# Kernel optimization log

Measured on AMD Instinct MI355X. Metric: run time of the kernel, lower is better.

## Reference

```python
import jax, jax.numpy as jnp
import numpy as np

# dims
B, C, H, W = 2, 64, 512, 512
T = 16                      # tile_size_l0
GH, GW = H // T, W // T
K = GH * GW                 # 1024 tiles
KMAX = 256                  # kmax_l0
HID = 2 * C
# routing config
THRESH = 0.0                # theta_on
TEMP = 1.0                  # gate_temperature
C_HEAVY, C_CHEAP = 1.0, 0.1
BUDGET_TOTAL = 512.0        # per-sample budget
MU = 1.0                    # dual controller multiplier (mu_init)


def setup_inputs() -> dict:
    key = jax.random.key(0)
    ks = jax.random.split(key, 6)
    sc = 0.05
    return {
        "dense_features": jax.random.normal(ks[0], (B, C, H, W), jnp.float32),
        "utility_logits": jax.random.normal(ks[1], (B, K), jnp.float32),
        "W1": jax.random.normal(ks[2], (C, HID), jnp.float32) * sc,
        "b1": jnp.zeros((HID,), jnp.float32),
        "W2": jax.random.normal(ks[3], (HID, C), jnp.float32) * sc,
        "b2": jnp.zeros((C,), jnp.float32),
        "Wa": jax.random.normal(ks[4], (C,), jnp.float32) * sc,
        "ba": jnp.zeros((1,), jnp.float32),
    }


def _select_mask(u):
    # vectorized equivalent of _select_from_gate: gate = u >= thresh,
    # keep top-KMAX gated tiles per sample ordered by utility.
    gate = u >= THRESH
    masked = jnp.where(gate, u, -1e30)
    vals, idx = jax.lax.top_k(masked, KMAX)          # [B,KMAX]
    valid = vals > -1e29
    rows = jnp.arange(u.shape[0])[:, None]
    return jnp.zeros(u.shape, bool).at[rows, idx].set(valid)  # [B,K]


def reference(dense_features, utility_logits, W1, b1, W2, b2, Wa, ba):
    x, u = dense_features, utility_logits
    # ste_gate_from_utilities (threshold mode)
    probabilities = jax.nn.sigmoid((u - THRESH) / TEMP)
    hard = (u >= THRESH).astype(x.dtype)
    gates = hard + probabilities - jax.lax.stop_gradient(probabilities)  # STE
    # tile selection (detached, like gates[b].detach())
    sel = _select_mask(jax.lax.stop_gradient(u))                 # [B,K]
    mask = sel.reshape(B, GH, GW).astype(x.dtype)
    mask = jnp.repeat(jnp.repeat(mask, T, axis=1), T, axis=2)[:, None]  # [B,1,H,W]
    # heavy path: pointwise channel MLP -> detail, alpha blend on selected tiles
    h = jax.nn.gelu(jnp.einsum('bchw,cd->bdhw', x, W1) + b1[None, :, None, None])
    detail = jnp.einsum('bdhw,dc->bchw', h, W2) + b2[None, :, None, None]
    alpha = jax.nn.sigmoid(jnp.einsum('bchw,c->bhw', x, Wa) + ba[0])[:, None]  # [B,1,H,W]
    alpha_out = mask * alpha
    detail_out = mask * detail
    heavy = x + alpha_out * detail
    # budget controller
    expected_cost = jnp.sum(probabilities * C_HEAVY + (1.0 - probabilities) * C_CHEAP)
    budget_loss = MU * jax.nn.relu(expected_cost - BUDGET_TOTAL * B)
    return heavy, detail_out, alpha_out, probabilities, gates, expected_cost, budget_loss
```

## Files before the change

kernel.cpp:

```cpp
#include <hip/hip_runtime.h>
#include <math.h>

#define Bv 2
#define Cv 64
#define Hv 512
#define Wv 512
#define Tv 16
#define Kv 1024
#define KMAXv 256
#define HIDv 128
#define HWv (Hv * Wv)

#define OFF_HEAVY 0
#define OFF_DETAIL 33554432
#define OFF_ALPHA 67108864
#define OFF_PROB 67633152
#define OFF_GATES 67635200
#define OFF_EC 67637248
#define OFF_BL 67637249

#define WS_SEL_OFF 0
#define WS_COST_OFF 8192

__global__ __launch_bounds__(1024) void sel_kernel(const float* __restrict__ u,
                                                   float* __restrict__ out,
                                                   int* __restrict__ selflag,
                                                   float* __restrict__ costp) {
    int b = blockIdx.x;
    int t = threadIdx.x;
    __shared__ float us[Kv];
    __shared__ float red[16];

    float ui = u[b * Kv + t];
    us[t] = ui;
    __syncthreads();

    float p = 1.0f / (1.0f + __expf(-ui));
    float hard = (ui >= 0.0f) ? 1.0f : 0.0f;
    out[OFF_PROB + b * Kv + t] = p;
    out[OFF_GATES + b * Kv + t] = (hard + p) - p;

    float cost = p + (1.0f - p) * 0.1f;
    #pragma unroll
    for (int o = 32; o > 0; o >>= 1) cost += __shfl_down(cost, o, 64);
    int wave = t >> 6, lane = t & 63;
    if (lane == 0) red[wave] = cost;
    __syncthreads();
    if (t == 0) {
        float s = 0.f;
        #pragma unroll
        for (int i = 0; i < 16; i++) s += red[i];
        costp[b] = s;
    }

    int selected = 0;
    if (ui >= 0.0f) {
        int r = 0;
        for (int j = 0; j < Kv; j += 4) {
            float4 uj = *(const float4*)&us[j];
            r += (uj.x > ui) || (uj.x == ui && (j + 0) < t);
            r += (uj.y > ui) || (uj.y == ui && (j + 1) < t);
            r += (uj.z > ui) || (uj.z == ui && (j + 2) < t);
            r += (uj.w > ui) || (uj.w == ui && (j + 3) < t);
        }
        selected = (r < KMAXv) ? 1 : 0;
    }
    selflag[b * Kv + t] = selected;
}

__global__ __launch_bounds__(256) void copy_kernel(const float* __restrict__ x,
                                                   float* __restrict__ out,
                                                   const int* __restrict__ selflag,
                                                   const float* __restrict__ costp) {
    int blk = blockIdx.x;
    int t = threadIdx.x;

    if (blk == 0 && t == 0) {
        float ec = costp[0] + costp[1];
        out[OFF_EC] = ec;
        out[OFF_BL] = (ec > 1024.0f) ? (ec - 1024.0f) : 0.0f;
    }

    if (selflag[blk]) return;

    int b = blk >> 10;
    int tile = blk & 1023;
    int gh = tile >> 5, gw = tile & 31;
    int h0 = gh * Tv, w0 = gw * Tv;

    int cplane = t >> 6;
    int r = (t >> 2) & 15;
    int q = t & 3;
    int base = ((b * Cv + cplane) * Hv + (h0 + r)) * Wv + w0 + q * 4;
    float4 z = make_float4(0.f, 0.f, 0.f, 0.f);
    #pragma unroll 4
    for (int c4 = 0; c4 < 16; c4++) {
        int idx = base + c4 * 4 * HWv;
        float4 v = *(const float4*)&x[idx];
        *(float4*)&out[OFF_HEAVY + idx] = v;
        *(float4*)&out[OFF_DETAIL + idx] = z;
    }
    if (t < 64) {
        int r2 = t >> 2, q2 = t & 3;
        int aidx = (b * Hv + h0 + r2) * Wv + w0 + q2 * 4;
        *(float4*)&out[OFF_ALPHA + aidx] = z;
    }
}

__global__ __launch_bounds__(256) void mlp_kernel(const float* __restrict__ x,
                                                  const float* __restrict__ W1,
                                                  const float* __restrict__ b1,
                                                  const float* __restrict__ W2,
                                                  const float* __restrict__ b2,
                                                  const float* __restrict__ Wa,
                                                  const float* __restrict__ ba,
                                                  float* __restrict__ out,
                                                  const int* __restrict__ selflag) {
    int blk = blockIdx.x;
    if (!selflag[blk]) return;

    __shared__ float xs[Cv][257];
    int t = threadIdx.x;
    int b = blk >> 10;
    int tile = blk & 1023;
    int gh = tile >> 5, gw = tile & 31;
    int h0 = gh * Tv, w0 = gw * Tv;

    int pr = t >> 4, pc = t & 15;
    int pbase = ((b * Cv) * Hv + (h0 + pr)) * Wv + w0 + pc;

    #pragma unroll 8
    for (int c = 0; c < Cv; c++) xs[c][t] = x[pbase + c * HWv];
    __syncthreads();

    float aacc = ba[0];
    #pragma unroll 8
    for (int c = 0; c < Cv; c++) aacc += xs[c][t] * Wa[c];
    float alpha = 1.0f / (1.0f + __expf(-aacc));
    out[OFF_ALPHA + (b * Hv + h0 + pr) * Wv + w0 + pc] = alpha;

    float D[Cv];
    #pragma unroll
    for (int c4 = 0; c4 < 16; c4++) {
        float4 bb = *(const float4*)&b2[c4 * 4];
        D[4 * c4 + 0] = bb.x; D[4 * c4 + 1] = bb.y;
        D[4 * c4 + 2] = bb.z; D[4 * c4 + 3] = bb.w;
    }

    for (int d0 = 0; d0 < HIDv; d0 += 32) {
        float Hc[32];
        #pragma unroll
        for (int j4 = 0; j4 < 8; j4++) {
            float4 bb = *(const float4*)&b1[d0 + 4 * j4];
            Hc[4 * j4 + 0] = bb.x; Hc[4 * j4 + 1] = bb.y;
            Hc[4 * j4 + 2] = bb.z; Hc[4 * j4 + 3] = bb.w;
        }
        #pragma unroll 2
        for (int c = 0; c < Cv; c++) {
            float xc = xs[c][t];
            const float4* w1p = (const float4*)(W1 + c * HIDv + d0);
            #pragma unroll
            for (int j4 = 0; j4 < 8; j4++) {
                float4 w = w1p[j4];
                Hc[4 * j4 + 0] += xc * w.x;
                Hc[4 * j4 + 1] += xc * w.y;
                Hc[4 * j4 + 2] += xc * w.z;
                Hc[4 * j4 + 3] += xc * w.w;
            }
        }
        #pragma unroll
        for (int j = 0; j < 32; j++) {
            float zv = Hc[j];
            float zz = 0.7978845608028654f * (zv + 0.044715f * zv * zv * zv);
            float e = __expf(2.0f * zz);
            float th = 1.0f - 2.0f / (e + 1.0f);
            Hc[j] = 0.5f * zv * (1.0f + th);
        }
        #pragma unroll 2
        for (int j = 0; j < 32; j++) {
            float hj = Hc[j];
            const float4* w2p = (const float4*)(W2 + (d0 + j) * Cv);
            #pragma unroll
            for (int c4 = 0; c4 < 16; c4++) {
                float4 w = w2p[c4];
                D[4 * c4 + 0] += hj * w.x;
                D[4 * c4 + 1] += hj * w.y;
                D[4 * c4 + 2] += hj * w.z;
                D[4 * c4 + 3] += hj * w.w;
            }
        }
    }

    #pragma unroll 4
    for (int c = 0; c < Cv; c++) {
        int idx = pbase + c * HWv;
        float det = D[c];
        out[OFF_DETAIL + idx] = det;
        out[OFF_HEAVY + idx] = xs[c][t] + alpha * det;
    }
}

extern "C" void kernel_launch(void* const* d_in, const int* in_sizes, int n_in,
                              void* d_out, int out_size, void* d_ws, size_t ws_size,
                              hipStream_t stream) {
    const float* x  = (const float*)d_in[0];
    const float* u  = (const float*)d_in[1];
    const float* W1 = (const float*)d_in[2];
    const float* b1 = (const float*)d_in[3];
    const float* W2 = (const float*)d_in[4];
    const float* b2 = (const float*)d_in[5];
    const float* Wa = (const float*)d_in[6];
    const float* ba = (const float*)d_in[7];
    float* out = (float*)d_out;

    char* ws = (char*)d_ws;
    int*   selflag = (int*)(ws + WS_SEL_OFF);
    float* costp   = (float*)(ws + WS_COST_OFF);

    sel_kernel<<<Bv, 1024, 0, stream>>>(u, out, selflag, costp);
    copy_kernel<<<Bv * Kv, 256, 0, stream>>>(x, out, selflag, costp);
    mlp_kernel<<<Bv * Kv, 256, 0, stream>>>(x, W1, b1, W2, b2, Wa, ba, out, selflag);
}
```

Measured before the change: 708.2 us.

## Fuse copy and MLP kernels into one launch over 8x32 half-tile-pair blocks

Merges the passthrough copy kernel and the MLP kernel into a single kernel. Each block now covers an 8-row by 32-column region spanning two horizontally adjacent tiles, so row accesses are wider and more coalesced. Mixed regions compute the MLP for every pixel and mask the outputs per tile. Shared-memory staging of x is replaced by re-reading x from global memory (through the cache) three times, and occupancy is hinted with launch_bounds(256,4). The cost is wasted MLP work on unselected halves of mixed pairs, plus extra global reads.

```diff
diff --git a/kernel.cpp b/kernel.cpp
--- a/kernel.cpp
+++ b/kernel.cpp
@@ -5,7 +5,6 @@
 #define Cv 64
 #define Hv 512
 #define Wv 512
-#define Tv 16
 #define Kv 1024
 #define KMAXv 256
 #define HIDv 128
@@ -68,10 +67,16 @@
     selflag[b * Kv + t] = selected;
 }
 
-__global__ __launch_bounds__(256) void copy_kernel(const float* __restrict__ x,
-                                                   float* __restrict__ out,
-                                                   const int* __restrict__ selflag,
-                                                   const float* __restrict__ costp) {
+__global__ __launch_bounds__(256, 4) void fused_kernel(const float* __restrict__ x,
+                                                       const float* __restrict__ W1,
+                                                       const float* __restrict__ b1,
+                                                       const float* __restrict__ W2,
+                                                       const float* __restrict__ b2,
+                                                       const float* __restrict__ Wa,
+                                                       const float* __restrict__ ba,
+                                                       float* __restrict__ out,
+                                                       const int* __restrict__ selflag,
+                                                       const float* __restrict__ costp) {
     int blk = blockIdx.x;
     int t = threadIdx.x;
 
@@ -81,63 +86,56 @@
         out[OFF_BL] = (ec > 1024.0f) ? (ec - 1024.0f) : 0.0f;
     }
 
-    if (selflag[blk]) return;
-
     int b = blk >> 10;
-    int tile = blk & 1023;
-    int gh = tile >> 5, gw = tile & 31;
-    int h0 = gh * Tv, w0 = gw * Tv;
-
-    int cplane = t >> 6;
-    int r = (t >> 2) & 15;
-    int q = t & 3;
-    int base = ((b * Cv + cplane) * Hv + (h0 + r)) * Wv + w0 + q * 4;
-    float4 z = make_float4(0.f, 0.f, 0.f, 0.f);
-    #pragma unroll 4
-    for (int c4 = 0; c4 < 16; c4++) {
-        int idx = base + c4 * 4 * HWv;
-        float4 v = *(const float4*)&x[idx];
-        *(float4*)&out[OFF_HEAVY + idx] = v;
-        *(float4*)&out[OFF_DETAIL + idx] = z;
-    }
-    if (t < 64) {
-        int r2 = t >> 2, q2 = t & 3;
-        int aidx = (b * Hv + h0 + r2) * Wv + w0 + q2 * 4;
-        *(float4*)&out[OFF_ALPHA + aidx] = z;
-    }
-}
-
-__global__ __launch_bounds__(256) void mlp_kernel(const float* __restrict__ x,
-                                                  const float* __restrict__ W1,
-                                                  const float* __restrict__ b1,
-                                                  const float* __restrict__ W2,
-                                                  const float* __restrict__ b2,
-                                                  const float* __restrict__ Wa,
-                                                  const float* __restrict__ ba,
-                                                  float* __restrict__ out,
-                                                  const int* __restrict__ selflag) {
-    int blk = blockIdx.x;
-    if (!selflag[blk]) return;
-
-    __shared__ float xs[Cv][257];
-    int t = threadIdx.x;
-    int b = blk >> 10;
-    int tile = blk & 1023;
-    int gh = tile >> 5, gw = tile & 31;
-    int h0 = gh * Tv, w0 = gw * Tv;
-
-    int pr = t >> 4, pc = t & 15;
-    int pbase = ((b * Cv) * Hv + (h0 + pr)) * Wv + w0 + pc;
-
-    #pragma unroll 8
-    for (int c = 0; c < Cv; c++) xs[c][t] = x[pbase + c * HWv];
-    __syncthreads();
+    int rem = blk & 1023;
+    int pairid = rem >> 1;
+    int half = rem & 1;
+    int gh = pairid >> 4;
+    int gp = pairid & 15;
+    int h0 = gh * 16 + half * 8;
+    int w0 = gp * 32;
+
+    int tA = b * Kv + gh * 32 + gp * 2;
+    int selA = selflag[tA];
+    int selB = selflag[tA + 1];
+
+    if ((selA | selB) == 0) {
+        int pl = t >> 6;
+        int r = (t >> 3) & 7;
+        int q = t & 7;
+        int base = ((b * Cv + pl) * Hv + h0 + r) * Wv + w0 + q * 4;
+        float4 z = make_float4(0.f, 0.f, 0.f, 0.f);
+        #pragma unroll 4
+        for (int it = 0; it < 16; it++) {
+            int idx = base + it * 4 * HWv;
+            float4 v = *(const float4*)&x[idx];
+            *(float4*)&out[OFF_HEAVY + idx] = v;
+            *(float4*)&out[OFF_DETAIL + idx] = z;
+        }
+        if (t < 64) {
+            int r2 = t >> 3, q2 = t & 7;
+            int aidx = (b * Hv + h0 + r2) * Wv + w0 + q2 * 4;
+            *(float4*)&out[OFF_ALPHA + aidx] = z;
+        }
+        return;
+    }
+
+    int r = t >> 5;
+    int cc = t & 31;
+    float msk = (cc < 16) ? (float)selA : (float)selB;
+    int pbase = (b * Cv * Hv + h0 + r) * Wv + w0 + cc;
 
     float aacc = ba[0];
-    #pragma unroll 8
-    for (int c = 0; c < Cv; c++) aacc += xs[c][t] * Wa[c];
+    for (int c0 = 0; c0 < Cv; c0 += 8) {
+        float xv[8];
+        #pragma unroll
+        for (int k = 0; k < 8; k++) xv[k] = x[pbase + (c0 + k) * HWv];
+        #pragma unroll
+        for (int k = 0; k < 8; k++) aacc += xv[k] * Wa[c0 + k];
+    }
     float alpha = 1.0f / (1.0f + __expf(-aacc));
-    out[OFF_ALPHA + (b * Hv + h0 + pr) * Wv + w0 + pc] = alpha;
+    float am = msk * alpha;
+    out[OFF_ALPHA + (b * Hv + h0 + r) * Wv + w0 + cc] = am;
 
     float D[Cv];
     #pragma unroll
@@ -155,17 +153,22 @@
             Hc[4 * j4 + 0] = bb.x; Hc[4 * j4 + 1] = bb.y;
             Hc[4 * j4 + 2] = bb.z; Hc[4 * j4 + 3] = bb.w;
         }
-        #pragma unroll 2
-        for (int c = 0; c < Cv; c++) {
-            float xc = xs[c][t];
-            const float4* w1p = (const float4*)(W1 + c * HIDv + d0);
+        for (int c0 = 0; c0 < Cv; c0 += 8) {
+            float xv[8];
             #pragma unroll
-            for (int j4 = 0; j4 < 8; j4++) {
-                float4 w = w1p[j4];
-                Hc[4 * j4 + 0] += xc * w.x;
-                Hc[4 * j4 + 1] += xc * w.y;
-                Hc[4 * j4 + 2] += xc * w.z;
-                Hc[4 * j4 + 3] += xc * w.w;
+            for (int k = 0; k < 8; k++) xv[k] = x[pbase + (c0 + k) * HWv];
+            #pragma unroll
+            for (int k = 0; k < 8; k++) {
+                float xc = xv[k];
+                const float4* w1p = (const float4*)(W1 + (c0 + k) * HIDv + d0);
+                #pragma unroll
+                for (int j4 = 0; j4 < 8; j4++) {
+                    float4 w = w1p[j4];
+                    Hc[4 * j4 + 0] += xc * w.x;
+                    Hc[4 * j4 + 1] += xc * w.y;
+                    Hc[4 * j4 + 2] += xc * w.z;
+                    Hc[4 * j4 + 3] += xc * w.w;
+                }
             }
         }
         #pragma unroll
@@ -176,7 +179,7 @@
             float th = 1.0f - 2.0f / (e + 1.0f);
             Hc[j] = 0.5f * zv * (1.0f + th);
         }
-        #pragma unroll 2
+        #pragma unroll 4
         for (int j = 0; j < 32; j++) {
             float hj = Hc[j];
             const float4* w2p = (const float4*)(W2 + (d0 + j) * Cv);
@@ -191,12 +194,17 @@
         }
     }
 
-    #pragma unroll 4
-    for (int c = 0; c < Cv; c++) {
-        int idx = pbase + c * HWv;
-        float det = D[c];
-        out[OFF_DETAIL + idx] = det;
-        out[OFF_HEAVY + idx] = xs[c][t] + alpha * det;
+    for (int c0 = 0; c0 < Cv; c0 += 8) {
+        float xv[8];
+        #pragma unroll
+        for (int k = 0; k < 8; k++) xv[k] = x[pbase + (c0 + k) * HWv];
+        #pragma unroll
+        for (int k = 0; k < 8; k++) {
+            int idx = pbase + (c0 + k) * HWv;
+            float det = D[c0 + k];
+            out[OFF_DETAIL + idx] = msk * det;
+            out[OFF_HEAVY + idx] = xv[k] + am * det;
+        }
     }
 }
 
@@ -218,6 +226,5 @@
     float* costp   = (float*)(ws + WS_COST_OFF);
 
     sel_kernel<<<Bv, 1024, 0, stream>>>(u, out, selflag, costp);
-    copy_kernel<<<Bv * Kv, 256, 0, stream>>>(x, out, selflag, costp);
-    mlp_kernel<<<Bv * Kv, 256, 0, stream>>>(x, W1, b1, W2, b2, Wa, ba, out, selflag);
+    fused_kernel<<<Bv * Kv, 256, 0, stream>>>(x, W1, b1, W2, b2, Wa, ba, out, selflag, costp);
 }
```

Result: slower. 1.683 ms (+137.6%).
